# Optimization experiments

Measured on AMD Instinct MI355X. Metric: run time of the kernel, lower is better.

Reference implementation:

```python
import jax, jax.numpy as jnp
import numpy as np
import math
from jax import lax

B, C, H, DK, L, K, NCONV, P = 24, 128, 8, 16, 512, 7, 4, 0.1


def setup_inputs() -> dict:
    key = jax.random.key(0)
    ks = jax.random.split(key, 10)
    return {
        "x": jax.random.normal(ks[0], (B, C, L), jnp.float32),
        "dw_w": jax.random.normal(ks[1], (NCONV, C, 1, K), jnp.float32) * 0.1,
        "dw_b": jax.random.normal(ks[2], (NCONV, C), jnp.float32) * 0.1,
        "pw_w": jax.random.normal(ks[3], (NCONV, C, C, 1), jnp.float32) * 0.05,
        "pw_b": jax.random.normal(ks[4], (NCONV, C), jnp.float32) * 0.1,
        "Wq": jax.random.normal(ks[5], (H, B, DK, C), jnp.float32),
        "Wk": jax.random.normal(ks[6], (H, B, DK, C), jnp.float32),
        "Wv": jax.random.normal(ks[7], (H, B, DK, C), jnp.float32),
        "Wo": jax.random.normal(ks[8], (B, C, C), jnp.float32),
        "W": jax.random.normal(ks[9], (B, C, C), jnp.float32),
    }


def _norm(t, eps=1e-6):
    # torch: (x - mean) / (std + eps), std unbiased (ddof=1), over last (length) axis
    mean = t.mean(-1, keepdims=True)
    std = jnp.sqrt(((t - mean) ** 2).sum(-1, keepdims=True) / (t.shape[-1] - 1))
    return (t - mean) / (std + eps)


def _dropout(t, i):
    # deterministic dropout (training=True, p=0.1) with fixed per-call key
    keep = jax.random.bernoulli(jax.random.fold_in(jax.random.key(7), i), 1.0 - P, t.shape)
    return jnp.where(keep, t / (1.0 - P), jnp.zeros((), t.dtype))


def reference(x, dw_w, dw_b, pw_w, pw_b, Wq, Wk, Wv, Wo, W):
    # positional encoding: sin(sin(pos*freq + phase)) + x (note the double sin, faithful to source)
    i = np.arange(C)
    base = 10000.0 ** (-(i - (i % 2)) / C)
    freq = jnp.asarray(np.where(i % 2 == 0, base, -base), jnp.float32)
    phase = jnp.asarray(np.where(i % 2 == 0, 0.0, np.pi / 2), jnp.float32)
    pos = jnp.arange(L, dtype=jnp.float32)
    pe = jnp.sin(jnp.sin(pos[None, :] * freq[:, None] + phase[:, None]))  # (C, L)
    out = pe[None] + x
    res = out
    dn = ('NCH', 'OIH', 'NCH')
    for ci in range(NCONV):
        o = _norm(out)
        o = lax.conv_general_dilated(o, dw_w[ci], (1,), [(K // 2, K // 2)],
                                     feature_group_count=C, dimension_numbers=dn) + dw_b[ci][None, :, None]
        o = lax.conv_general_dilated(o, pw_w[ci], (1,), [(0, 0)],
                                     dimension_numbers=dn) + pw_b[ci][None, :, None]
        o = jax.nn.relu(o)
        out = _dropout(res + o, ci)
        res = out
    # self-attention (per-batch-element weight matrices, softmax over QUERY axis = torch dim=1)
    xn = _norm(out)
    q = jnp.einsum('hbkc,bcl->hbkl', Wq, xn)
    k = jnp.einsum('hbkc,bcl->hbkl', Wk, xn)
    v = jnp.einsum('hbkc,bcl->hbkl', Wv, xn)
    s = jnp.einsum('hbki,hbkj->hbij', q, k) / math.sqrt(DK)  # (H,B,L,L)
    p = jax.nn.softmax(s, axis=2)
    head = jnp.einsum('hbvi,hbij->hbvj', v, p)  # (H,B,DK,L)
    head = head.transpose(1, 0, 2, 3).reshape(B, H * DK, L)
    att = jnp.einsum('boc,bcl->bol', Wo, head)
    out = _dropout(res + att, NCONV)
    res = out
    # final per-batch projection + relu + residual
    o = jax.nn.relu(jnp.einsum('boc,bcl->bol', W, _norm(out)))
    out = _dropout(res + o, NCONV + 1)
    return out
```

## Files before the change

### kernel.cpp

```cpp
#include <hip/hip_runtime.h>
#include <stdint.h>
#include <math.h>

#define NB 24
#define NC 128
#define NH 8
#define NDK 16
#define NL 512
#define NTOT (24*128*512)

typedef float f32x4 __attribute__((ext_vector_type(4)));
typedef short s16x4 __attribute__((ext_vector_type(4)));

__device__ inline f32x4 mfma_bf16_16x16x16(s16x4 a, s16x4 b, f32x4 c) {
#if defined(__HIP_DEVICE_COMPILE__)
#if __has_builtin(__builtin_amdgcn_mfma_f32_16x16x16bf16_1k)
  return __builtin_amdgcn_mfma_f32_16x16x16bf16_1k(a, b, c, 0, 0, 0);
#else
  return __builtin_amdgcn_mfma_f32_16x16x16_bf16(a, b, c, 0, 0, 0);
#endif
#else
  (void)a; (void)b;
  return c;
#endif
}

__device__ inline unsigned short f2bf(float x) {
  uint32_t u = __float_as_uint(x);
  return (unsigned short)((u + 0x7FFFu + ((u >> 16) & 1u)) >> 16);
}
__device__ inline float bf2f(unsigned short s) {
  return __uint_as_float(((uint32_t)s) << 16);
}

__host__ __device__ inline void tf2x32(uint32_t k0, uint32_t k1, uint32_t& x0, uint32_t& x1) {
  uint32_t ks2 = k0 ^ k1 ^ 0x1BD11BDAu;
  x0 += k0; x1 += k1;
#define TF_R(r) { x0 += x1; x1 = (x1 << r) | (x1 >> (32 - r)); x1 ^= x0; }
  TF_R(13) TF_R(15) TF_R(26) TF_R(6)
  x0 += k1;  x1 += ks2 + 1u;
  TF_R(17) TF_R(29) TF_R(16) TF_R(24)
  x0 += ks2; x1 += k0 + 2u;
  TF_R(13) TF_R(15) TF_R(26) TF_R(6)
  x0 += k0;  x1 += k1 + 3u;
  TF_R(17) TF_R(29) TF_R(16) TF_R(24)
  x0 += k1;  x1 += ks2 + 4u;
  TF_R(13) TF_R(15) TF_R(26) TF_R(6)
  x0 += ks2; x1 += k0 + 5u;
#undef TF_R
}

__device__ inline float drop_scale(uint32_t k0, uint32_t k1, uint32_t idx) {
  uint32_t x0 = 0u, x1 = idx;
  tf2x32(k0, k1, x0, x1);
  uint32_t bits = x0 ^ x1;
  float u = __uint_as_float((bits >> 9) | 0x3f800000u) - 1.0f;
  return (u < 0.9f) ? (1.0f / 0.9f) : 0.0f;
}

__global__ __launch_bounds__(256) void pos_add_kernel(const float* __restrict__ x,
                                                      float* __restrict__ out) {
  int idx = blockIdx.x * 256 + threadIdx.x;
  int l = idx & (NL - 1);
  int c = (idx >> 9) & (NC - 1);
  int ce = c & ~1;
  double base = exp(-(double)ce * 9.210340371976184 / 128.0);
  float freq = (c & 1) ? -(float)base : (float)base;
  float phase = (c & 1) ? (float)(M_PI / 2.0) : 0.0f;
  float pe = sinf(sinf((float)l * freq + phase));
  out[idx] = x[idx] + pe;
}

template<bool DO_CONV>
__global__ __launch_bounds__(64) void norm_dw_kernel(const float* __restrict__ in,
                                                     float* __restrict__ outp,
                                                     const float* __restrict__ dww,
                                                     const float* __restrict__ dwb) {
  int row = blockIdx.x;
  int c = row & (NC - 1);
  int t = threadIdx.x;
  const float* rp = in + (size_t)row * NL;
  float4 v0 = ((const float4*)rp)[t * 2];
  float4 v1 = ((const float4*)rp)[t * 2 + 1];
  float xr[8] = {v0.x, v0.y, v0.z, v0.w, v1.x, v1.y, v1.z, v1.w};
  float s = 0.f;
#pragma unroll
  for (int j = 0; j < 8; ++j) s += xr[j];
#pragma unroll
  for (int off = 32; off >= 1; off >>= 1) s += __shfl_xor(s, off);
  float mean = s * (1.0f / 512.0f);
  float sq = 0.f;
#pragma unroll
  for (int j = 0; j < 8; ++j) { xr[j] -= mean; sq += xr[j] * xr[j]; }
#pragma unroll
  for (int off = 32; off >= 1; off >>= 1) sq += __shfl_xor(sq, off);
  float inv = 1.0f / (sqrtf(sq * (1.0f / 511.0f)) + 1e-6f);

  if (!DO_CONV) {
    float4 o0 = make_float4(xr[0]*inv, xr[1]*inv, xr[2]*inv, xr[3]*inv);
    float4 o1 = make_float4(xr[4]*inv, xr[5]*inv, xr[6]*inv, xr[7]*inv);
    float4* op = (float4*)(outp + (size_t)row * NL);
    op[t * 2] = o0; op[t * 2 + 1] = o1;
  } else {
    __shared__ float rb[NL + 6];
    if (t < 3) { rb[t] = 0.f; rb[NL + 3 + t] = 0.f; }
#pragma unroll
    for (int j = 0; j < 8; ++j) rb[3 + t * 8 + j] = xr[j] * inv;
    __syncthreads();
    float w[7];
#pragma unroll
    for (int u = 0; u < 7; ++u) w[u] = dww[c * 7 + u];
    float bias = dwb[c];
    float* op = outp + (size_t)row * NL + t * 8;
#pragma unroll
    for (int j = 0; j < 8; ++j) {
      int l = t * 8 + j;
      float o = bias;
#pragma unroll
      for (int u = 0; u < 7; ++u) o += rb[l + u] * w[u];
      op[j] = o;
    }
  }
}

template<int EPI, bool A_PER_B>
__global__ __launch_bounds__(256) void gemm128_kernel(const float* __restrict__ A,
                                                      const float* __restrict__ X,
                                                      float* __restrict__ Y,
                                                      const float* __restrict__ bias,
                                                      const float* __restrict__ resid,
                                                      uint32_t k0, uint32_t k1) {
  __shared__ float As[64][129];
  __shared__ float Xs[128][68];
  int b  = blockIdx.z;
  int m0 = blockIdx.y * 64;
  int l0 = blockIdx.x * 64;
  int t  = threadIdx.x;
  const float* Ab = A + (A_PER_B ? (size_t)b * NC * NC : 0);
  const float* Xb = X + (size_t)b * NC * NL;

#pragma unroll
  for (int i = 0; i < 8; ++i) {
    int id = t + i * 256;
    int r = id >> 5;
    int c4 = (id & 31) << 2;
    float4 v = *(const float4*)&Ab[(size_t)(m0 + r) * NC + c4];
    As[r][c4] = v.x; As[r][c4+1] = v.y; As[r][c4+2] = v.z; As[r][c4+3] = v.w;
  }
#pragma unroll
  for (int i = 0; i < 8; ++i) {
    int id = t + i * 256;
    int r = id >> 4;
    int c4 = (id & 15) << 2;
    float4 v = *(const float4*)&Xb[(size_t)r * NL + l0 + c4];
    Xs[r][c4] = v.x; Xs[r][c4+1] = v.y; Xs[r][c4+2] = v.z; Xs[r][c4+3] = v.w;
  }
  __syncthreads();

  int tm = t >> 4, tl = t & 15;
  float acc[4][4] = {};
#pragma unroll 4
  for (int k = 0; k < 128; ++k) {
    float a0 = As[tm*4+0][k], a1 = As[tm*4+1][k], a2 = As[tm*4+2][k], a3 = As[tm*4+3][k];
    float4 xv = *(const float4*)&Xs[k][tl << 2];
    acc[0][0] += a0*xv.x; acc[0][1] += a0*xv.y; acc[0][2] += a0*xv.z; acc[0][3] += a0*xv.w;
    acc[1][0] += a1*xv.x; acc[1][1] += a1*xv.y; acc[1][2] += a1*xv.z; acc[1][3] += a1*xv.w;
    acc[2][0] += a2*xv.x; acc[2][1] += a2*xv.y; acc[2][2] += a2*xv.z; acc[2][3] += a2*xv.w;
    acc[3][0] += a3*xv.x; acc[3][1] += a3*xv.y; acc[3][2] += a3*xv.z; acc[3][3] += a3*xv.w;
  }

#pragma unroll
  for (int i = 0; i < 4; ++i) {
    int m = m0 + tm * 4 + i;
    float bv = (EPI == 0) ? bias[m] : 0.0f;
#pragma unroll
    for (int j = 0; j < 4; ++j) {
      int l = l0 + tl * 4 + j;
      float val = acc[i][j] + bv;
      if (EPI == 0 || EPI == 2) val = fmaxf(val, 0.0f);
      size_t idx = ((size_t)b * NC + m) * NL + l;
      float v2 = resid[idx] + val;
      float ds = drop_scale(k0, k1, (uint32_t)idx);
      Y[idx] = (ds == 0.0f) ? 0.0f : (v2 / 0.9f);
    }
  }
}

__global__ __launch_bounds__(256) void qkv_kernel(const float* __restrict__ Wq,
                                                  const float* __restrict__ Wk,
                                                  const float* __restrict__ Wv,
                                                  const float* __restrict__ X,
                                                  unsigned short* __restrict__ qhw,
                                                  unsigned short* __restrict__ qlw,
                                                  unsigned short* __restrict__ khw,
                                                  unsigned short* __restrict__ klw,
                                                  unsigned short* __restrict__ vbw) {
  __shared__ float As[64][129];
  __shared__ float Xs[128][68];
  int b  = blockIdx.z;
  int m0 = blockIdx.y * 64;
  int l0 = blockIdx.x * 64;
  int t  = threadIdx.x;
  const float* Xb = X + (size_t)b * NC * NL;

#pragma unroll
  for (int i = 0; i < 8; ++i) {
    int id = t + i * 256;
    int r = id >> 5;
    int c4 = (id & 31) << 2;
    int gr = m0 + r;
    int sel = gr >> 7, w = gr & 127, h = w >> 4, kk = w & 15;
    const float* Wp = (sel == 0) ? Wq : ((sel == 1) ? Wk : Wv);
    const float* rowp = Wp + (((size_t)h * NB + b) * NDK + kk) * NC;
    float4 v = *(const float4*)&rowp[c4];
    As[r][c4] = v.x; As[r][c4+1] = v.y; As[r][c4+2] = v.z; As[r][c4+3] = v.w;
  }
#pragma unroll
  for (int i = 0; i < 8; ++i) {
    int id = t + i * 256;
    int r = id >> 4;
    int c4 = (id & 15) << 2;
    float4 v = *(const float4*)&Xb[(size_t)r * NL + l0 + c4];
    Xs[r][c4] = v.x; Xs[r][c4+1] = v.y; Xs[r][c4+2] = v.z; Xs[r][c4+3] = v.w;
  }
  __syncthreads();

  int tm = t >> 4, tl = t & 15;
  float acc[4][4] = {};
#pragma unroll 4
  for (int k = 0; k < 128; ++k) {
    float a0 = As[tm*4+0][k], a1 = As[tm*4+1][k], a2 = As[tm*4+2][k], a3 = As[tm*4+3][k];
    float4 xv = *(const float4*)&Xs[k][tl << 2];
    acc[0][0] += a0*xv.x; acc[0][1] += a0*xv.y; acc[0][2] += a0*xv.z; acc[0][3] += a0*xv.w;
    acc[1][0] += a1*xv.x; acc[1][1] += a1*xv.y; acc[1][2] += a1*xv.z; acc[1][3] += a1*xv.w;
    acc[2][0] += a2*xv.x; acc[2][1] += a2*xv.y; acc[2][2] += a2*xv.z; acc[2][3] += a2*xv.w;
    acc[3][0] += a3*xv.x; acc[3][1] += a3*xv.y; acc[3][2] += a3*xv.z; acc[3][3] += a3*xv.w;
  }

#pragma unroll
  for (int i = 0; i < 4; ++i) {
    int gr = m0 + tm * 4 + i;
    int sel = gr >> 7, w = gr & 127, h = w >> 4, kk = w & 15;
    size_t base = (((size_t)h * NB + b) * NDK + kk) * NL + l0 + tl * 4;
#pragma unroll
    for (int j = 0; j < 4; ++j) {
      float v = acc[i][j];
      size_t idx = base + j;
      if (sel == 0) {
        float s = v * 0.25f;
        unsigned short hi = f2bf(s);
        qhw[idx] = hi; qlw[idx] = f2bf(s - bf2f(hi));
      } else if (sel == 1) {
        unsigned short hi = f2bf(v);
        khw[idx] = hi; klw[idx] = f2bf(v - bf2f(hi));
      } else {
        vbw[idx] = f2bf(v);
      }
    }
  }
}

__global__ __launch_bounds__(256) void attn_kernel(const unsigned short* __restrict__ qh,
                                                   const unsigned short* __restrict__ ql,
                                                   const unsigned short* __restrict__ kh,
                                                   const unsigned short* __restrict__ kl,
                                                   const unsigned short* __restrict__ vb,
                                                   float* __restrict__ headbuf) {
  __shared__ unsigned short KtH[128][16], KtL[128][16];
  __shared__ unsigned short QtH[2][16][16], QtL[2][16][16], Vt[2][16][16];
  const int t = threadIdx.x;
  const int lane = t & 63, w = t >> 6;
  const int g = lane >> 4, j16 = lane & 15;
  const int hb = blockIdx.y, jq = blockIdx.x;
  const int j0 = jq * 128;
  const int h = hb / NB, b = hb % NB;
  const size_t kb = (size_t)hb * NDK * NL;

  {
    int j = t & 127, k8 = (t >> 7) * 8;
#pragma unroll
    for (int kk = 0; kk < 8; ++kk) {
      KtH[j][k8 + kk] = kh[kb + (size_t)(k8 + kk) * NL + j0 + j];
      KtL[j][k8 + kk] = kl[kb + (size_t)(k8 + kk) * NL + j0 + j];
    }
  }
  {
    int k_ = t >> 4, i_ = t & 15;
    size_t src = kb + (size_t)k_ * NL + i_;
    QtH[0][i_][k_] = qh[src];
    QtL[0][i_][k_] = ql[src];
    Vt [0][k_][i_] = vb[src];
  }
  __syncthreads();

  s16x4 KhiF[2], KloF[2];
#pragma unroll
  for (int q = 0; q < 2; ++q) {
    int jj = (w * 2 + q) * 16 + j16;
    KhiF[q] = *(const s16x4*)&KtH[jj][4 * g];
    KloF[q] = *(const s16x4*)&KtL[jj][4 * g];
  }

  float Mq[2] = {-INFINITY, -INFINITY};
  float lq[2] = {0.f, 0.f};
  f32x4 hC[2] = {{0.f, 0.f, 0.f, 0.f}, {0.f, 0.f, 0.f, 0.f}};

  int buf = 0;
  for (int it = 0; it < 32; ++it) {
    if (it < 31) {
      int k_ = t >> 4, i_ = t & 15, nb = buf ^ 1;
      size_t src = kb + (size_t)k_ * NL + (it + 1) * 16 + i_;
      QtH[nb][i_][k_] = qh[src];
      QtL[nb][i_][k_] = ql[src];
      Vt [nb][k_][i_] = vb[src];
    }
    s16x4 Qhi = *(const s16x4*)&QtH[buf][j16][4 * g];
    s16x4 Qlo = *(const s16x4*)&QtL[buf][j16][4 * g];
    s16x4 Vf  = *(const s16x4*)&Vt [buf][j16][4 * g];
#pragma unroll
    for (int q = 0; q < 2; ++q) {
      f32x4 S = {0.f, 0.f, 0.f, 0.f};
      S = mfma_bf16_16x16x16(Qhi, KhiF[q], S);
      S = mfma_bf16_16x16x16(Qlo, KhiF[q], S);
      S = mfma_bf16_16x16x16(Qhi, KloF[q], S);
      float tm = fmaxf(fmaxf(S[0], S[1]), fmaxf(S[2], S[3]));
      tm = fmaxf(tm, __shfl_xor(tm, 16));
      tm = fmaxf(tm, __shfl_xor(tm, 32));
      float Mn = fmaxf(Mq[q], tm);
      float corr = __expf(Mq[q] - Mn);
      Mq[q] = Mn;
      float p0 = __expf(S[0] - Mn), p1 = __expf(S[1] - Mn);
      float p2 = __expf(S[2] - Mn), p3 = __expf(S[3] - Mn);
      lq[q] = lq[q] * corr + ((p0 + p1) + (p2 + p3));
      hC[q] = hC[q] * corr;
      union { uint32_t u[2]; s16x4 s; } bp;
      bp.u[0] = (uint32_t)f2bf(p0) | ((uint32_t)f2bf(p1) << 16);
      bp.u[1] = (uint32_t)f2bf(p2) | ((uint32_t)f2bf(p3) << 16);
      hC[q] = mfma_bf16_16x16x16(Vf, bp.s, hC[q]);
    }
    __syncthreads();
    buf ^= 1;
  }

#pragma unroll
  for (int q = 0; q < 2; ++q) {
    float l2 = lq[q] + __shfl_xor(lq[q], 16);
    float L  = l2 + __shfl_xor(l2, 32);
    float invL = 1.0f / L;
    int jglob = j0 + (w * 2 + q) * 16 + j16;
    float* hp = headbuf + ((size_t)b * NC + h * NDK + 4 * g) * NL + jglob;
    hp[0 * NL] = hC[q][0] * invL;
    hp[1 * NL] = hC[q][1] * invL;
    hp[2 * NL] = hC[q][2] * invL;
    hp[3 * NL] = hC[q][3] * invL;
  }
}

extern "C" void kernel_launch(void* const* d_in, const int* in_sizes, int n_in,
                              void* d_out, int out_size, void* d_ws, size_t ws_size,
                              hipStream_t stream) {
  (void)in_sizes; (void)n_in; (void)out_size; (void)ws_size;
  const float* x    = (const float*)d_in[0];
  const float* dw_w = (const float*)d_in[1];
  const float* dw_b = (const float*)d_in[2];
  const float* pw_w = (const float*)d_in[3];
  const float* pw_b = (const float*)d_in[4];
  const float* Wq   = (const float*)d_in[5];
  const float* Wk   = (const float*)d_in[6];
  const float* Wv   = (const float*)d_in[7];
  const float* Wo   = (const float*)d_in[8];
  const float* W    = (const float*)d_in[9];
  float* out = (float*)d_out;

  const size_t N = NTOT;
  float* cur  = (float*)d_ws;
  float* bufA = cur + N;
  float* bufB = bufA + N;
  unsigned short* qh = (unsigned short*)(bufB + N);
  unsigned short* ql = qh + N;
  unsigned short* kh = ql + N;
  unsigned short* kl = kh + N;
  unsigned short* vb = kl + N;

  uint32_t fk0[6], fk1[6];
  for (int i = 0; i < 6; ++i) {
    uint32_t a = 0u, bb = (uint32_t)i;
    tf2x32(0u, 7u, a, bb);
    fk0[i] = a; fk1[i] = bb;
  }

  pos_add_kernel<<<NTOT / 256, 256, 0, stream>>>(x, cur);

  for (int ci = 0; ci < 4; ++ci) {
    norm_dw_kernel<true><<<NB * NC, 64, 0, stream>>>(cur, bufB, dw_w + ci * NC * 7, dw_b + ci * NC);
    gemm128_kernel<0, false><<<dim3(8, 2, NB), 256, 0, stream>>>(
        pw_w + (size_t)ci * NC * NC, bufB, cur, pw_b + ci * NC, cur, fk0[ci], fk1[ci]);
  }

  norm_dw_kernel<false><<<NB * NC, 64, 0, stream>>>(cur, bufA, nullptr, nullptr);
  qkv_kernel<<<dim3(8, 6, NB), 256, 0, stream>>>(Wq, Wk, Wv, bufA, qh, ql, kh, kl, vb);
  attn_kernel<<<dim3(4, NH * NB), 256, 0, stream>>>(qh, ql, kh, kl, vb, bufB);
  gemm128_kernel<1, true><<<dim3(8, 2, NB), 256, 0, stream>>>(
      Wo, bufB, cur, nullptr, cur, fk0[4], fk1[4]);

  norm_dw_kernel<false><<<NB * NC, 64, 0, stream>>>(cur, bufA, nullptr, nullptr);
  gemm128_kernel<2, true><<<dim3(8, 2, NB), 256, 0, stream>>>(
      W, bufA, out, nullptr, cur, fk0[5], fk1[5]);
}
```

Before: 211.6 us.

## Switch pointwise and QKV GEMMs to split-bf16 MFMA with K-chunked staging

Replaces the scalar FP32 64x64 GEMM tiles in the pointwise, output-projection and QKV kernels with bf16 MFMA 16x16x16 instructions. Each FP32 operand is split into hi and lo bf16 parts and three MFMAs approximate FP32 accuracy. K is staged through LDS in two 64-wide chunks, and X is stored transposed so the MFMA B operand can be read as contiguous vectors. The aim is to cut the FMA-bound inner loop, at the cost of conversion work, strided scalar global loads for X, and some precision loss from dropping the lo*lo term.

```diff
diff --git a/kernel.cpp b/kernel.cpp
--- a/kernel.cpp
+++ b/kernel.cpp
@@ -124,61 +124,75 @@
 }
 
 template<int EPI, bool A_PER_B>
-__global__ __launch_bounds__(256) void gemm128_kernel(const float* __restrict__ A,
-                                                      const float* __restrict__ X,
-                                                      float* __restrict__ Y,
-                                                      const float* __restrict__ bias,
-                                                      const float* __restrict__ resid,
-                                                      uint32_t k0, uint32_t k1) {
-  __shared__ float As[64][129];
-  __shared__ float Xs[128][68];
+__global__ __launch_bounds__(256) void gemm_mfma_kernel(const float* __restrict__ A,
+                                                        const float* __restrict__ X,
+                                                        float* __restrict__ Y,
+                                                        const float* __restrict__ bias,
+                                                        const float* __restrict__ resid,
+                                                        uint32_t k0, uint32_t k1) {
+  __shared__ unsigned short Ah[64][68], Al[64][68];
+  __shared__ unsigned short Xh[64][68], Xl[64][68];
   int b  = blockIdx.z;
   int m0 = blockIdx.y * 64;
   int l0 = blockIdx.x * 64;
   int t  = threadIdx.x;
+  const int lane = t & 63, w = t >> 6;
+  const int g = lane >> 4, j16 = lane & 15;
   const float* Ab = A + (A_PER_B ? (size_t)b * NC * NC : 0);
   const float* Xb = X + (size_t)b * NC * NL;
 
-#pragma unroll
-  for (int i = 0; i < 8; ++i) {
-    int id = t + i * 256;
-    int r = id >> 5;
-    int c4 = (id & 31) << 2;
-    float4 v = *(const float4*)&Ab[(size_t)(m0 + r) * NC + c4];
-    As[r][c4] = v.x; As[r][c4+1] = v.y; As[r][c4+2] = v.z; As[r][c4+3] = v.w;
-  }
-#pragma unroll
-  for (int i = 0; i < 8; ++i) {
-    int id = t + i * 256;
-    int r = id >> 4;
-    int c4 = (id & 15) << 2;
-    float4 v = *(const float4*)&Xb[(size_t)r * NL + l0 + c4];
-    Xs[r][c4] = v.x; Xs[r][c4+1] = v.y; Xs[r][c4+2] = v.z; Xs[r][c4+3] = v.w;
-  }
-  __syncthreads();
-
-  int tm = t >> 4, tl = t & 15;
-  float acc[4][4] = {};
-#pragma unroll 4
-  for (int k = 0; k < 128; ++k) {
-    float a0 = As[tm*4+0][k], a1 = As[tm*4+1][k], a2 = As[tm*4+2][k], a3 = As[tm*4+3][k];
-    float4 xv = *(const float4*)&Xs[k][tl << 2];
-    acc[0][0] += a0*xv.x; acc[0][1] += a0*xv.y; acc[0][2] += a0*xv.z; acc[0][3] += a0*xv.w;
-    acc[1][0] += a1*xv.x; acc[1][1] += a1*xv.y; acc[1][2] += a1*xv.z; acc[1][3] += a1*xv.w;
-    acc[2][0] += a2*xv.x; acc[2][1] += a2*xv.y; acc[2][2] += a2*xv.z; acc[2][3] += a2*xv.w;
-    acc[3][0] += a3*xv.x; acc[3][1] += a3*xv.y; acc[3][2] += a3*xv.z; acc[3][3] += a3*xv.w;
-  }
-
-#pragma unroll
-  for (int i = 0; i < 4; ++i) {
-    int m = m0 + tm * 4 + i;
-    float bv = (EPI == 0) ? bias[m] : 0.0f;
-#pragma unroll
-    for (int j = 0; j < 4; ++j) {
-      int l = l0 + tl * 4 + j;
-      float val = acc[i][j] + bv;
+  f32x4 acc[4] = {{0.f,0.f,0.f,0.f},{0.f,0.f,0.f,0.f},{0.f,0.f,0.f,0.f},{0.f,0.f,0.f,0.f}};
+
+  for (int kc = 0; kc < 2; ++kc) {
+#pragma unroll
+    for (int i = 0; i < 4; ++i) {
+      int id = t + i * 256;
+      int r = id >> 4, c4 = (id & 15) << 2;
+      float4 v = *(const float4*)&Ab[(size_t)(m0 + r) * NC + kc * 64 + c4];
+      unsigned short h0 = f2bf(v.x), h1 = f2bf(v.y), h2 = f2bf(v.z), h3 = f2bf(v.w);
+      Ah[r][c4] = h0; Ah[r][c4+1] = h1; Ah[r][c4+2] = h2; Ah[r][c4+3] = h3;
+      Al[r][c4]   = f2bf(v.x - bf2f(h0));
+      Al[r][c4+1] = f2bf(v.y - bf2f(h1));
+      Al[r][c4+2] = f2bf(v.z - bf2f(h2));
+      Al[r][c4+3] = f2bf(v.w - bf2f(h3));
+    }
+    {
+      int n = t & 63, kbase = (t >> 6) * 16;
+#pragma unroll
+      for (int kk = 0; kk < 16; ++kk) {
+        float v = Xb[(size_t)(kc * 64 + kbase + kk) * NL + l0 + n];
+        unsigned short hi = f2bf(v);
+        Xh[n][kbase + kk] = hi;
+        Xl[n][kbase + kk] = f2bf(v - bf2f(hi));
+      }
+    }
+    __syncthreads();
+#pragma unroll
+    for (int ks = 0; ks < 4; ++ks) {
+      int ko = ks * 16 + 4 * g;
+      s16x4 a_h = *(const s16x4*)&Ah[w * 16 + j16][ko];
+      s16x4 a_l = *(const s16x4*)&Al[w * 16 + j16][ko];
+#pragma unroll
+      for (int nt = 0; nt < 4; ++nt) {
+        s16x4 x_h = *(const s16x4*)&Xh[nt * 16 + j16][ko];
+        s16x4 x_l = *(const s16x4*)&Xl[nt * 16 + j16][ko];
+        acc[nt] = mfma_bf16_16x16x16(a_h, x_h, acc[nt]);
+        acc[nt] = mfma_bf16_16x16x16(a_l, x_h, acc[nt]);
+        acc[nt] = mfma_bf16_16x16x16(a_h, x_l, acc[nt]);
+      }
+    }
+    __syncthreads();
+  }
+
+#pragma unroll
+  for (int nt = 0; nt < 4; ++nt) {
+    int n = l0 + nt * 16 + j16;
+#pragma unroll
+    for (int r = 0; r < 4; ++r) {
+      int m = m0 + w * 16 + 4 * g + r;
+      float val = acc[nt][r] + ((EPI == 0) ? bias[m] : 0.0f);
       if (EPI == 0 || EPI == 2) val = fmaxf(val, 0.0f);
-      size_t idx = ((size_t)b * NC + m) * NL + l;
+      size_t idx = ((size_t)b * NC + m) * NL + n;
       float v2 = resid[idx] + val;
       float ds = drop_scale(k0, k1, (uint32_t)idx);
       Y[idx] = (ds == 0.0f) ? 0.0f : (v2 / 0.9f);
@@ -186,66 +200,82 @@
   }
 }
 
-__global__ __launch_bounds__(256) void qkv_kernel(const float* __restrict__ Wq,
-                                                  const float* __restrict__ Wk,
-                                                  const float* __restrict__ Wv,
-                                                  const float* __restrict__ X,
-                                                  unsigned short* __restrict__ qhw,
-                                                  unsigned short* __restrict__ qlw,
-                                                  unsigned short* __restrict__ khw,
-                                                  unsigned short* __restrict__ klw,
-                                                  unsigned short* __restrict__ vbw) {
-  __shared__ float As[64][129];
-  __shared__ float Xs[128][68];
+__global__ __launch_bounds__(256) void qkv_mfma_kernel(const float* __restrict__ Wq,
+                                                       const float* __restrict__ Wk,
+                                                       const float* __restrict__ Wv,
+                                                       const float* __restrict__ X,
+                                                       unsigned short* __restrict__ qhw,
+                                                       unsigned short* __restrict__ qlw,
+                                                       unsigned short* __restrict__ khw,
+                                                       unsigned short* __restrict__ klw,
+                                                       unsigned short* __restrict__ vbw) {
+  __shared__ unsigned short Ah[64][68], Al[64][68];
+  __shared__ unsigned short Xh[64][68], Xl[64][68];
   int b  = blockIdx.z;
   int m0 = blockIdx.y * 64;
   int l0 = blockIdx.x * 64;
   int t  = threadIdx.x;
+  const int lane = t & 63, w = t >> 6;
+  const int g = lane >> 4, j16 = lane & 15;
+  const int sel = m0 >> 7;
+  const float* Wp = (sel == 0) ? Wq : ((sel == 1) ? Wk : Wv);
   const float* Xb = X + (size_t)b * NC * NL;
 
-#pragma unroll
-  for (int i = 0; i < 8; ++i) {
-    int id = t + i * 256;
-    int r = id >> 5;
-    int c4 = (id & 31) << 2;
-    int gr = m0 + r;
-    int sel = gr >> 7, w = gr & 127, h = w >> 4, kk = w & 15;
-    const float* Wp = (sel == 0) ? Wq : ((sel == 1) ? Wk : Wv);
-    const float* rowp = Wp + (((size_t)h * NB + b) * NDK + kk) * NC;
-    float4 v = *(const float4*)&rowp[c4];
-    As[r][c4] = v.x; As[r][c4+1] = v.y; As[r][c4+2] = v.z; As[r][c4+3] = v.w;
-  }
-#pragma unroll
-  for (int i = 0; i < 8; ++i) {
-    int id = t + i * 256;
-    int r = id >> 4;
-    int c4 = (id & 15) << 2;
-    float4 v = *(const float4*)&Xb[(size_t)r * NL + l0 + c4];
-    Xs[r][c4] = v.x; Xs[r][c4+1] = v.y; Xs[r][c4+2] = v.z; Xs[r][c4+3] = v.w;
-  }
-  __syncthreads();
-
-  int tm = t >> 4, tl = t & 15;
-  float acc[4][4] = {};
-#pragma unroll 4
-  for (int k = 0; k < 128; ++k) {
-    float a0 = As[tm*4+0][k], a1 = As[tm*4+1][k], a2 = As[tm*4+2][k], a3 = As[tm*4+3][k];
-    float4 xv = *(const float4*)&Xs[k][tl << 2];
-    acc[0][0] += a0*xv.x; acc[0][1] += a0*xv.y; acc[0][2] += a0*xv.z; acc[0][3] += a0*xv.w;
-    acc[1][0] += a1*xv.x; acc[1][1] += a1*xv.y; acc[1][2] += a1*xv.z; acc[1][3] += a1*xv.w;
-    acc[2][0] += a2*xv.x; acc[2][1] += a2*xv.y; acc[2][2] += a2*xv.z; acc[2][3] += a2*xv.w;
-    acc[3][0] += a3*xv.x; acc[3][1] += a3*xv.y; acc[3][2] += a3*xv.z; acc[3][3] += a3*xv.w;
-  }
-
-#pragma unroll
-  for (int i = 0; i < 4; ++i) {
-    int gr = m0 + tm * 4 + i;
-    int sel = gr >> 7, w = gr & 127, h = w >> 4, kk = w & 15;
-    size_t base = (((size_t)h * NB + b) * NDK + kk) * NL + l0 + tl * 4;
-#pragma unroll
-    for (int j = 0; j < 4; ++j) {
-      float v = acc[i][j];
-      size_t idx = base + j;
+  f32x4 acc[4] = {{0.f,0.f,0.f,0.f},{0.f,0.f,0.f,0.f},{0.f,0.f,0.f,0.f},{0.f,0.f,0.f,0.f}};
+
+  for (int kc = 0; kc < 2; ++kc) {
+#pragma unroll
+    for (int i = 0; i < 4; ++i) {
+      int id = t + i * 256;
+      int r = id >> 4, c4 = (id & 15) << 2;
+      int gr = m0 + r;
+      int w_ = gr & 127, h = w_ >> 4, kk = w_ & 15;
+      const float* rowp = Wp + (((size_t)h * NB + b) * NDK + kk) * NC + kc * 64;
+      float4 v = *(const float4*)&rowp[c4];
+      unsigned short h0 = f2bf(v.x), h1 = f2bf(v.y), h2 = f2bf(v.z), h3 = f2bf(v.w);
+      Ah[r][c4] = h0; Ah[r][c4+1] = h1; Ah[r][c4+2] = h2; Ah[r][c4+3] = h3;
+      Al[r][c4]   = f2bf(v.x - bf2f(h0));
+      Al[r][c4+1] = f2bf(v.y - bf2f(h1));
+      Al[r][c4+2] = f2bf(v.z - bf2f(h2));
+      Al[r][c4+3] = f2bf(v.w - bf2f(h3));
+    }
+    {
+      int n = t & 63, kbase = (t >> 6) * 16;
+#pragma unroll
+      for (int kk = 0; kk < 16; ++kk) {
+        float v = Xb[(size_t)(kc * 64 + kbase + kk) * NL + l0 + n];
+        unsigned short hi = f2bf(v);
+        Xh[n][kbase + kk] = hi;
+        Xl[n][kbase + kk] = f2bf(v - bf2f(hi));
+      }
+    }
+    __syncthreads();
+#pragma unroll
+    for (int ks = 0; ks < 4; ++ks) {
+      int ko = ks * 16 + 4 * g;
+      s16x4 a_h = *(const s16x4*)&Ah[w * 16 + j16][ko];
+      s16x4 a_l = *(const s16x4*)&Al[w * 16 + j16][ko];
+#pragma unroll
+      for (int nt = 0; nt < 4; ++nt) {
+        s16x4 x_h = *(const s16x4*)&Xh[nt * 16 + j16][ko];
+        s16x4 x_l = *(const s16x4*)&Xl[nt * 16 + j16][ko];
+        acc[nt] = mfma_bf16_16x16x16(a_h, x_h, acc[nt]);
+        acc[nt] = mfma_bf16_16x16x16(a_l, x_h, acc[nt]);
+        acc[nt] = mfma_bf16_16x16x16(a_h, x_l, acc[nt]);
+      }
+    }
+    __syncthreads();
+  }
+
+#pragma unroll
+  for (int nt = 0; nt < 4; ++nt) {
+    int n = l0 + nt * 16 + j16;
+#pragma unroll
+    for (int r = 0; r < 4; ++r) {
+      int grow = m0 + w * 16 + 4 * g + r;
+      int w_ = grow & 127, h = w_ >> 4, kk = w_ & 15;
+      size_t idx = (((size_t)h * NB + b) * NDK + kk) * NL + n;
+      float v = acc[nt][r];
       if (sel == 0) {
         float s = v * 0.25f;
         unsigned short hi = f2bf(s);
@@ -393,17 +423,17 @@
 
   for (int ci = 0; ci < 4; ++ci) {
     norm_dw_kernel<true><<<NB * NC, 64, 0, stream>>>(cur, bufB, dw_w + ci * NC * 7, dw_b + ci * NC);
-    gemm128_kernel<0, false><<<dim3(8, 2, NB), 256, 0, stream>>>(
+    gemm_mfma_kernel<0, false><<<dim3(8, 2, NB), 256, 0, stream>>>(
         pw_w + (size_t)ci * NC * NC, bufB, cur, pw_b + ci * NC, cur, fk0[ci], fk1[ci]);
   }
 
   norm_dw_kernel<false><<<NB * NC, 64, 0, stream>>>(cur, bufA, nullptr, nullptr);
-  qkv_kernel<<<dim3(8, 6, NB), 256, 0, stream>>>(Wq, Wk, Wv, bufA, qh, ql, kh, kl, vb);
+  qkv_mfma_kernel<<<dim3(8, 6, NB), 256, 0, stream>>>(Wq, Wk, Wv, bufA, qh, ql, kh, kl, vb);
   attn_kernel<<<dim3(4, NH * NB), 256, 0, stream>>>(qh, ql, kh, kl, vb, bufB);
-  gemm128_kernel<1, true><<<dim3(8, 2, NB), 256, 0, stream>>>(
+  gemm_mfma_kernel<1, true><<<dim3(8, 2, NB), 256, 0, stream>>>(
       Wo, bufB, cur, nullptr, cur, fk0[4], fk1[4]);
 
   norm_dw_kernel<false><<<NB * NC, 64, 0, stream>>>(cur, bufA, nullptr, nullptr);
-  gemm128_kernel<2, true><<<dim3(8, 2, NB), 256, 0, stream>>>(
+  gemm_mfma_kernel<2, true><<<dim3(8, 2, NB), 256, 0, stream>>>(
       W, bufA, out, nullptr, cur, fk0[5], fk1[5]);
 }
```

Result: no change. 208.3 us (-1.6%).
